# Kernel tuning notes

Measured on AMD Instinct MI355X. Metric: run time of the kernel, lower is better.

## Reference

```python
import jax, jax.numpy as jnp
import numpy as np

EPS = 1e-6  # LayerNorm epsilon


def setup_inputs() -> dict:
    key = jax.random.key(0)
    ks = jax.random.split(key, 12)
    B, S, T, E = 8, 2048, 2048, 512
    sc = 1.0 / np.sqrt(E)
    inp = {
        "encoder_outputs": jax.random.normal(ks[0], (B, S, E), jnp.float32),
        "emotion": jax.random.normal(ks[1], (B, T, E), jnp.float32),
        "mask": jax.random.randint(ks[2], (B, S, T), 0, 2).astype(bool),
        "Wq": jax.random.normal(ks[3], (E, E), jnp.float32) * sc,
        "bq": jnp.zeros((E,), jnp.float32),
        "Wk": jax.random.normal(ks[4], (E, E), jnp.float32) * sc,
        "bk": jnp.zeros((E,), jnp.float32),
        "Wv": jax.random.normal(ks[5], (E, E), jnp.float32) * sc,
        "bv": jnp.zeros((E,), jnp.float32),
        "Wo": jax.random.normal(ks[6], (E, E), jnp.float32) * sc,
        "gamma": jnp.ones((E,), jnp.float32),
        "beta": jnp.zeros((E,), jnp.float32),
    }
    return inp


def reference(encoder_outputs, emotion, mask, Wq, bq, Wk, bk, Wv, bv, Wo, gamma, beta):
    # Linear projections (torch Linear: x @ W.T + b)
    q = encoder_outputs @ Wq.T + bq          # [B,S,E]
    k = emotion @ Wk.T + bk                  # [B,T,E]
    v = emotion @ Wv.T + bv                  # [B,T,E]
    logits = jnp.einsum("bse,bte->bst", q, k)  # [B,S,T]
    logits = jnp.where(mask, jnp.float32(-1e18), logits)
    weights = jax.nn.softmax(logits, axis=-1)   # dropout1 = identity (eval)
    contexts = jnp.einsum("bst,bte->bse", weights, v)
    attn = contexts @ Wo.T                   # output_linear, no bias
    attn = encoder_outputs + attn            # dropout2 = identity (eval)
    # LayerNorm (std-based, as in common hand-rolled LayerNorm)
    mean = attn.mean(-1, keepdims=True)
    std = attn.std(-1, keepdims=True)
    context = gamma * (attn - mean) / (std + EPS) + beta
    context = encoder_outputs + context      # dropout3 = identity (eval)
    return context
```

## Files before the change

kernel.cpp:

```cpp
#include <hip/hip_runtime.h>
#include <math.h>
#include <stdint.h>


#define BB 8
#define SS 2048
#define TT 2048
#define EE 512

typedef __attribute__((ext_vector_type(8))) short short8;
typedef __attribute__((ext_vector_type(4))) float f32x4;

__device__ __forceinline__ uint16_t f2bf(float f) {
  uint32_t u = __builtin_bit_cast(uint32_t, f);
  u += 0x7fffu + ((u >> 16) & 1u);
  return (uint16_t)(u >> 16);
}
__device__ __forceinline__ float bf2f(uint16_t h) {
  uint32_t u = ((uint32_t)h) << 16;
  return __builtin_bit_cast(float, u);
}

__device__ __forceinline__ size_t toff(int row, int col, int ld) {
  return (size_t)(row >> 4) * ((size_t)ld << 4) + ((size_t)(col >> 3) << 7)
       + ((row & 15) << 3) + (col & 7);
}

__device__ __forceinline__ void gld16(const void* g, void* l) {
  __builtin_amdgcn_global_load_lds(
      (const __attribute__((address_space(1))) void*)g,
      (__attribute__((address_space(3))) void*)l, 16, 0, 0);
}

template<int ASRC, int BSRC, int EPI, int WN>
__global__ __launch_bounds__(256, 2) void mgemm(
    const void* __restrict__ Ap, const void* __restrict__ Alo,
    const void* __restrict__ Bp, const void* __restrict__ Blo,
    void* __restrict__ Cp, void* __restrict__ C2,
    const float* __restrict__ bias, const float* __restrict__ resid,
    const int* __restrict__ mask, float* __restrict__ sZ,
    int K, int lda, int ldb, int ldc,
    size_t sA, size_t sB, size_t sC, size_t sM)
{
  constexpr bool ALOARR = (ASRC == 0);
  constexpr bool BLOARR = (BSRC == 0);
  constexpr bool T3     = (ASRC == 0) && (BSRC == 0);
  constexpr int  BN     = 32 * WN;
  constexpr int  ABYTES = ALOARR ? 16384 : 8192;
  constexpr int  BBYTES = BLOARR ? BN * 128 : BN * 64;

  __shared__ char smem[ABYTES + BBYTES];

  const int tid  = threadIdx.x;
  const int lane = tid & 63, wv = tid >> 6;
  const int z    = blockIdx.z;
  const int bm   = blockIdx.y * 128;
  const int bn   = blockIdx.x * BN;
  const int fr   = lane & 15;
  const int wm   = (wv & 1) * 64;
  const int wn   = (wv >> 1) * (16 * WN);

  const f32x4 zero = {0.f, 0.f, 0.f, 0.f};
  f32x4 acc[4][WN];
#pragma unroll
  for (int i = 0; i < 4; ++i)
#pragma unroll
    for (int j = 0; j < WN; ++j) acc[i][j] = zero;

  const size_t loff = (size_t)lane * 8;
  const uint16_t* gAh = (const uint16_t*)Ap + sA * z + (size_t)(bm >> 4) * 16 * lda + loff;
  const uint16_t* gAl = ALOARR ? (const uint16_t*)Alo + sA * z + (size_t)(bm >> 4) * 16 * lda + loff : nullptr;
  const uint16_t* gBh = (const uint16_t*)Bp + sB * z + (size_t)(bn >> 4) * 16 * ldb + loff;
  const uint16_t* gBl = BLOARR ? (const uint16_t*)Blo + sB * z + (size_t)(bn >> 4) * 16 * ldb + loff : nullptr;

  for (int k0 = 0; k0 < K; k0 += 32) {
    const size_t ka = (size_t)k0 * 16;
    __syncthreads();
#pragma unroll
    for (int t = 0; t < 2; ++t) { int s = wv + t * 4;
      gld16(gAh + (size_t)s * 16 * lda + ka, &smem[s * 1024]); }
    if constexpr (ALOARR) {
#pragma unroll
      for (int t = 0; t < 2; ++t) { int s = wv + t * 4;
        gld16(gAl + (size_t)s * 16 * lda + ka, &smem[8192 + s * 1024]); }
    }
#pragma unroll
    for (int t = 0; t < WN / 2; ++t) { int s = wv + t * 4;
      gld16(gBh + (size_t)s * 16 * ldb + ka, &smem[ABYTES + s * 1024]); }
    if constexpr (BLOARR) {
#pragma unroll
      for (int t = 0; t < WN / 2; ++t) { int s = wv + t * 4;
        gld16(gBl + (size_t)s * 16 * ldb + ka, &smem[ABYTES + BN * 64 + s * 1024]); }
    }
    __syncthreads();

    short8 ah[4], bh[WN], al_[4], bl_[WN];
#pragma unroll
    for (int i = 0; i < 4; ++i) {
      const char* p = smem + ((wm >> 4) + i) * 1024 + (lane << 4);
      ah[i] = *(const short8*)p;
      if constexpr (ALOARR) al_[i] = *(const short8*)(p + 8192);
    }
#pragma unroll
    for (int j = 0; j < WN; ++j) {
      const char* p = smem + ABYTES + ((wn >> 4) + j) * 1024 + (lane << 4);
      bh[j] = *(const short8*)p;
      if constexpr (BLOARR) bl_[j] = *(const short8*)(p + BN * 64);
    }
#pragma unroll
    for (int i = 0; i < 4; ++i)
#pragma unroll
      for (int j = 0; j < WN; ++j) {
        acc[i][j] = __builtin_amdgcn_mfma_f32_16x16x32_bf16(ah[i], bh[j], acc[i][j], 0, 0, 0);
        if constexpr (T3) {
          acc[i][j] = __builtin_amdgcn_mfma_f32_16x16x32_bf16(ah[i], bl_[j], acc[i][j], 0, 0, 0);
          acc[i][j] = __builtin_amdgcn_mfma_f32_16x16x32_bf16(al_[i], bh[j], acc[i][j], 0, 0, 0);
        }
      }
  }

  if constexpr (EPI == 5) {
#pragma unroll
    for (int i = 0; i < 4; ++i) {
      const int row0 = bm + wm + i * 16 + (lane >> 4) * 4;
#pragma unroll
      for (int g = 0; g < 4; ++g) {
        const int row = row0 + g;
        float rs = 0.f;
#pragma unroll
        for (int j = 0; j < WN; ++j) {
          const int col = bn + wn + j * 16 + fr;
          const bool msk = mask[sM * z + (size_t)row * ldc + col] != 0;
          const float e = msk ? 0.f : __expf(acc[i][j][g] - 60.0f);
          ((uint16_t*)Cp)[sC * z + toff(row, col, ldc)] = f2bf(e);
          rs += e;
        }
        rs += __shfl_xor(rs, 1);
        rs += __shfl_xor(rs, 2);
        rs += __shfl_xor(rs, 4);
        rs += __shfl_xor(rs, 8);
        if ((lane & 15) == 0) atomicAdd(&sZ[(size_t)z * SS + row], rs);
      }
    }
  } else {
#pragma unroll
    for (int i = 0; i < 4; ++i) {
      const int row0 = bm + wm + i * 16 + (lane >> 4) * 4;
#pragma unroll
      for (int g = 0; g < 4; ++g) {
        const int row = row0 + g;
        float invZ = 1.0f;
        if constexpr (EPI == 6) invZ = 1.0f / sZ[(size_t)z * SS + row];
#pragma unroll
        for (int j = 0; j < WN; ++j) {
          const int col = bn + wn + j * 16 + fr;
          float v = acc[i][j][g];
          if constexpr (EPI == 0) {
            const size_t ci = sC * z + toff(row, col, ldc);
            v += bias[col];
            uint16_t h = f2bf(v);
            ((uint16_t*)Cp)[ci] = h;
            ((uint16_t*)C2)[ci] = f2bf(v - bf2f(h));
          } else if constexpr (EPI == 1) {
            v += bias[row];
            ((uint16_t*)Cp)[sC * z + toff(row, col, ldc)] = f2bf(v);
          } else if constexpr (EPI == 4) {
            v += resid[(size_t)row * ldc + col];
            ((float*)Cp)[sC * z + (size_t)row * ldc + col] = v;
          } else {
            ((uint16_t*)Cp)[sC * z + toff(row, col, ldc)] = f2bf(v * invZ);
          }
        }
      }
    }
  }
}

__global__ __launch_bounds__(256) void split_tiled(
    const float* __restrict__ x, uint16_t* __restrict__ hi,
    uint16_t* __restrict__ lo)
{
  __shared__ uint16_t lh[256 * 8 + 16 * 8];
  __shared__ uint16_t ll[256 * 8 + 16 * 8];
  const int t   = threadIdx.x;
  const int seg = blockIdx.x >> 2, q = blockIdx.x & 3;

  const float* src = x + (size_t)(seg * 16 + (t >> 4)) * 512 + q * 128 + (t & 15) * 8;
  float4 a = *(const float4*)src;
  float4 b = *(const float4*)(src + 4);
  float v[8] = {a.x, a.y, a.z, a.w, b.x, b.y, b.z, b.w};

  const int slot = (t & 15) * 16 + (t >> 4);
  uint16_t* ph = lh + slot * 8 + (slot >> 4) * 8;
  uint16_t* pl = ll + slot * 8 + (slot >> 4) * 8;
#pragma unroll
  for (int e = 0; e < 8; ++e) {
    uint16_t h = f2bf(v[e]);
    ph[e] = h;
    pl[e] = f2bf(v[e] - bf2f(h));
  }
  __syncthreads();

  const uint16_t* qh = lh + t * 8 + (t >> 4) * 8;
  const uint16_t* ql = ll + t * 8 + (t >> 4) * 8;
  const size_t off = (size_t)seg * 8192 + (size_t)(q * 16 + (t >> 4)) * 128 + (t & 15) * 8;
  *(short8*)(hi + off) = *(const short8*)qh;
  *(short8*)(lo + off) = *(const short8*)ql;
}

__global__ __launch_bounds__(256) void ln_kernel(
    const float* __restrict__ X, const float* __restrict__ enc,
    const float* __restrict__ gamma, const float* __restrict__ beta,
    float* __restrict__ out)
{
  const int row = blockIdx.x * 4 + (threadIdx.x >> 6);
  const int lane = threadIdx.x & 63;
  const size_t base = (size_t)row * EE;
  const int o0 = lane * 4, o1 = 256 + lane * 4;

  float4 x0 = *(const float4*)(X + base + o0);
  float4 x1 = *(const float4*)(X + base + o1);
  float s = x0.x + x0.y + x0.z + x0.w + x1.x + x1.y + x1.z + x1.w;
#pragma unroll
  for (int off = 32; off > 0; off >>= 1) s += __shfl_xor(s, off);
  const float mean = s * (1.0f / 512.0f);

  float d[8] = {x0.x - mean, x0.y - mean, x0.z - mean, x0.w - mean,
                x1.x - mean, x1.y - mean, x1.z - mean, x1.w - mean};
  float s2 = 0.f;
#pragma unroll
  for (int i = 0; i < 8; ++i) s2 = fmaf(d[i], d[i], s2);
#pragma unroll
  for (int off = 32; off > 0; off >>= 1) s2 += __shfl_xor(s2, off);
  const float stdv = sqrtf(s2 * (1.0f / 512.0f));
  const float inv = 1.0f / (stdv + 1e-6f);

  float4 g0 = *(const float4*)(gamma + o0);
  float4 g1 = *(const float4*)(gamma + o1);
  float4 b0 = *(const float4*)(beta + o0);
  float4 b1 = *(const float4*)(beta + o1);
  float4 e0 = *(const float4*)(enc + base + o0);
  float4 e1 = *(const float4*)(enc + base + o1);

  float4 r0, r1;
  r0.x = e0.x + g0.x * d[0] * inv + b0.x;
  r0.y = e0.y + g0.y * d[1] * inv + b0.y;
  r0.z = e0.z + g0.z * d[2] * inv + b0.z;
  r0.w = e0.w + g0.w * d[3] * inv + b0.w;
  r1.x = e1.x + g1.x * d[4] * inv + b1.x;
  r1.y = e1.y + g1.y * d[5] * inv + b1.y;
  r1.z = e1.z + g1.z * d[6] * inv + b1.z;
  r1.w = e1.w + g1.w * d[7] * inv + b1.w;
  *(float4*)(out + base + o0) = r0;
  *(float4*)(out + base + o1) = r1;
}

extern "C" void kernel_launch(void* const* d_in, const int* in_sizes, int n_in,
                              void* d_out, int out_size, void* d_ws, size_t ws_size,
                              hipStream_t stream) {
  const float* enc   = (const float*)d_in[0];
  const float* emo   = (const float*)d_in[1];
  const int*   mask  = (const int*)d_in[2];
  const float* Wq    = (const float*)d_in[3];
  const float* bq    = (const float*)d_in[4];
  const float* Wk    = (const float*)d_in[5];
  const float* bk    = (const float*)d_in[6];
  const float* Wv    = (const float*)d_in[7];
  const float* bv    = (const float*)d_in[8];
  const float* Wo    = (const float*)d_in[9];
  const float* gamma = (const float*)d_in[10];
  const float* beta  = (const float*)d_in[11];
  float* out = (float*)d_out;
  char*  ws  = (char*)d_ws;

  const size_t SZ = (size_t)BB * SS * EE;
  size_t off = 0;
  uint16_t* enc_h = (uint16_t*)(ws + off); off += SZ * 2;
  uint16_t* enc_l = (uint16_t*)(ws + off); off += SZ * 2;
  uint16_t* emo_h = (uint16_t*)(ws + off); off += SZ * 2;
  uint16_t* emo_l = (uint16_t*)(ws + off); off += SZ * 2;
  uint16_t* q_hi  = (uint16_t*)(ws + off); off += SZ * 2;
  uint16_t* q_lo  = (uint16_t*)(ws + off); off += SZ * 2;
  uint16_t* k_hi  = (uint16_t*)(ws + off); off += SZ * 2;
  uint16_t* k_lo  = (uint16_t*)(ws + off); off += SZ * 2;
  uint16_t* vT    = (uint16_t*)(ws + off); off += SZ * 2;
  uint16_t* ctx   = (uint16_t*)(ws + off); off += SZ * 2;
  uint16_t* wq_h  = (uint16_t*)(ws + off); off += EE * EE * 2;
  uint16_t* wq_l  = (uint16_t*)(ws + off); off += EE * EE * 2;
  uint16_t* wk_h  = (uint16_t*)(ws + off); off += EE * EE * 2;
  uint16_t* wk_l  = (uint16_t*)(ws + off); off += EE * EE * 2;
  uint16_t* wv_h  = (uint16_t*)(ws + off); off += EE * EE * 2;
  uint16_t* wv_l  = (uint16_t*)(ws + off); off += EE * EE * 2;
  uint16_t* wo_h  = (uint16_t*)(ws + off); off += EE * EE * 2;
  uint16_t* wo_l  = (uint16_t*)(ws + off); off += EE * EE * 2;
  uint16_t* P_u   = (uint16_t*)(ws + off); off += (size_t)BB * SS * TT * 2;
  float*    sZ    = (float*)(ws + off);    off += (size_t)BB * SS * 4;

  const dim3 blk(256);

  split_tiled<<<dim3(128),  blk, 0, stream>>>(Wq, wq_h, wq_l);
  split_tiled<<<dim3(128),  blk, 0, stream>>>(Wk, wk_h, wk_l);
  split_tiled<<<dim3(128),  blk, 0, stream>>>(Wv, wv_h, wv_l);
  split_tiled<<<dim3(128),  blk, 0, stream>>>(Wo, wo_h, wo_l);
  split_tiled<<<dim3(4096), blk, 0, stream>>>(enc, enc_h, enc_l);
  split_tiled<<<dim3(4096), blk, 0, stream>>>(emo, emo_h, emo_l);
  hipMemsetAsync(sZ, 0, (size_t)BB * SS * 4, stream);

  mgemm<0, 0, 0, 4><<<dim3(4, 128, 1), blk, 0, stream>>>(
      enc_h, enc_l, wq_h, wq_l, q_hi, q_lo, bq, nullptr, nullptr, nullptr,
      EE, EE, EE, EE, 0, 0, 0, 0);
  mgemm<0, 0, 0, 4><<<dim3(4, 128, 1), blk, 0, stream>>>(
      emo_h, emo_l, wk_h, wk_l, k_hi, k_lo, bk, nullptr, nullptr, nullptr,
      EE, EE, EE, EE, 0, 0, 0, 0);
  mgemm<1, 1, 1, 4><<<dim3(128, 4, 1), blk, 0, stream>>>(
      wv_h, nullptr, emo_h, nullptr, vT, nullptr, bv, nullptr, nullptr, nullptr,
      EE, EE, EE, BB * TT, 0, 0, 0, 0);

  mgemm<0, 0, 5, 4><<<dim3(16, 16, 8), blk, 0, stream>>>(
      q_hi, q_lo, k_hi, k_lo, P_u, nullptr, nullptr, nullptr, mask, sZ,
      EE, EE, EE, TT,
      (size_t)SS * EE, (size_t)TT * EE, (size_t)SS * TT, (size_t)SS * TT);

  mgemm<1, 1, 6, 4><<<dim3(4, 16, 8), blk, 0, stream>>>(
      P_u, nullptr, vT, nullptr, ctx, nullptr, nullptr, nullptr, nullptr, sZ,
      TT, TT, BB * TT, EE,
      (size_t)SS * TT, (size_t)TT * 16, (size_t)SS * EE, 0);

  mgemm<1, 1, 4, 4><<<dim3(4, 128, 1), blk, 0, stream>>>(
      ctx, nullptr, wo_h, nullptr, out, nullptr, nullptr, enc, nullptr, nullptr,
      EE, EE, EE, EE, 0, 0, 0, 0);
  ln_kernel<<<dim3(BB * SS / 4), blk, 0, stream>>>(out, enc, gamma, beta, out);
}
```

Baseline: 577.9 us.

## Batch split and Q/K projection launches, drop K low-part term in logits

Merges the four weight-split launches into one kernel and the two activation-split launches into another. The Q and K projections become a single batched GEMM launch, with per-z bias selection, relying on the workspace buffers being laid out contiguously. The QK^T logits GEMM now uses two bf16 MFMA terms instead of three by dropping K's low part, which cuts MFMA work and K-lo loads in the largest GEMM. The cost is slightly lower logit precision and a dependency on the workspace layout.

```diff
diff --git a/kernel.cpp b/kernel.cpp
--- a/kernel.cpp
+++ b/kernel.cpp
@@ -37,7 +37,8 @@
     const void* __restrict__ Ap, const void* __restrict__ Alo,
     const void* __restrict__ Bp, const void* __restrict__ Blo,
     void* __restrict__ Cp, void* __restrict__ C2,
-    const float* __restrict__ bias, const float* __restrict__ resid,
+    const float* __restrict__ bias, const float* __restrict__ bias2,
+    const float* __restrict__ resid,
     const int* __restrict__ mask, float* __restrict__ sZ,
     int K, int lda, int ldb, int ldc,
     size_t sA, size_t sB, size_t sC, size_t sM)
@@ -45,6 +46,7 @@
   constexpr bool ALOARR = (ASRC == 0);
   constexpr bool BLOARR = (BSRC == 0);
   constexpr bool T3     = (ASRC == 0) && (BSRC == 0);
+  constexpr bool T2     = (ASRC == 0) && (BSRC == 1);
   constexpr int  BN     = 32 * WN;
   constexpr int  ABYTES = ALOARR ? 16384 : 8192;
   constexpr int  BBYTES = BLOARR ? BN * 128 : BN * 64;
@@ -114,6 +116,8 @@
         acc[i][j] = __builtin_amdgcn_mfma_f32_16x16x32_bf16(ah[i], bh[j], acc[i][j], 0, 0, 0);
         if constexpr (T3) {
           acc[i][j] = __builtin_amdgcn_mfma_f32_16x16x32_bf16(ah[i], bl_[j], acc[i][j], 0, 0, 0);
+          acc[i][j] = __builtin_amdgcn_mfma_f32_16x16x32_bf16(al_[i], bh[j], acc[i][j], 0, 0, 0);
+        } else if constexpr (T2) {
           acc[i][j] = __builtin_amdgcn_mfma_f32_16x16x32_bf16(al_[i], bh[j], acc[i][j], 0, 0, 0);
         }
       }
@@ -156,8 +160,9 @@
           const int col = bn + wn + j * 16 + fr;
           float v = acc[i][j][g];
           if constexpr (EPI == 0) {
+            const float* bp = (z == 0) ? bias : bias2;
             const size_t ci = sC * z + toff(row, col, ldc);
-            v += bias[col];
+            v += bp[col];
             uint16_t h = f2bf(v);
             ((uint16_t*)Cp)[ci] = h;
             ((uint16_t*)C2)[ci] = f2bf(v - bf2f(h));
@@ -176,14 +181,14 @@
   }
 }
 
-__global__ __launch_bounds__(256) void split_tiled(
+__device__ __forceinline__ void split_core(
     const float* __restrict__ x, uint16_t* __restrict__ hi,
-    uint16_t* __restrict__ lo)
+    uint16_t* __restrict__ lo, int bid)
 {
   __shared__ uint16_t lh[256 * 8 + 16 * 8];
   __shared__ uint16_t ll[256 * 8 + 16 * 8];
   const int t   = threadIdx.x;
-  const int seg = blockIdx.x >> 2, q = blockIdx.x & 3;
+  const int seg = bid >> 2, q = bid & 3;
 
   const float* src = x + (size_t)(seg * 16 + (t >> 4)) * 512 + q * 128 + (t & 15) * 8;
   float4 a = *(const float4*)src;
@@ -206,6 +211,26 @@
   const size_t off = (size_t)seg * 8192 + (size_t)(q * 16 + (t >> 4)) * 128 + (t & 15) * 8;
   *(short8*)(hi + off) = *(const short8*)qh;
   *(short8*)(lo + off) = *(const short8*)ql;
+}
+
+__global__ __launch_bounds__(256) void split_pair(
+    const float* __restrict__ x0, const float* __restrict__ x1,
+    uint16_t* __restrict__ hi, uint16_t* __restrict__ lo, size_t stride)
+{
+  const int sel = blockIdx.x >> 12;
+  const int bid = blockIdx.x & 4095;
+  split_core(sel ? x1 : x0, hi + sel * stride, lo + sel * stride, bid);
+}
+
+__global__ __launch_bounds__(256) void split_w4(
+    const float* __restrict__ x0, const float* __restrict__ x1,
+    const float* __restrict__ x2, const float* __restrict__ x3,
+    uint16_t* __restrict__ hi0, uint16_t* __restrict__ lo0, size_t stride)
+{
+  const int w   = blockIdx.x >> 7;
+  const int bid = blockIdx.x & 127;
+  const float* x = (w == 0) ? x0 : (w == 1) ? x1 : (w == 2) ? x2 : x3;
+  split_core(x, hi0 + w * stride, lo0 + w * stride, bid);
 }
 
 __global__ __launch_bounds__(256) void ln_kernel(
@@ -295,39 +320,35 @@
   uint16_t* wo_l  = (uint16_t*)(ws + off); off += EE * EE * 2;
   uint16_t* P_u   = (uint16_t*)(ws + off); off += (size_t)BB * SS * TT * 2;
   float*    sZ    = (float*)(ws + off);    off += (size_t)BB * SS * 4;
+  (void)k_lo; (void)wk_l; (void)wv_l; (void)wo_l;
 
   const dim3 blk(256);
 
-  split_tiled<<<dim3(128),  blk, 0, stream>>>(Wq, wq_h, wq_l);
-  split_tiled<<<dim3(128),  blk, 0, stream>>>(Wk, wk_h, wk_l);
-  split_tiled<<<dim3(128),  blk, 0, stream>>>(Wv, wv_h, wv_l);
-  split_tiled<<<dim3(128),  blk, 0, stream>>>(Wo, wo_h, wo_l);
-  split_tiled<<<dim3(4096), blk, 0, stream>>>(enc, enc_h, enc_l);
-  split_tiled<<<dim3(4096), blk, 0, stream>>>(emo, emo_h, emo_l);
+  split_w4<<<dim3(512), blk, 0, stream>>>(Wq, Wk, Wv, Wo, wq_h, wq_l,
+                                          (size_t)2 * EE * EE);
+  split_pair<<<dim3(8192), blk, 0, stream>>>(enc, emo, enc_h, enc_l,
+                                             (size_t)2 * SZ);
   hipMemsetAsync(sZ, 0, (size_t)BB * SS * 4, stream);
 
-  mgemm<0, 0, 0, 4><<<dim3(4, 128, 1), blk, 0, stream>>>(
-      enc_h, enc_l, wq_h, wq_l, q_hi, q_lo, bq, nullptr, nullptr, nullptr,
-      EE, EE, EE, EE, 0, 0, 0, 0);
-  mgemm<0, 0, 0, 4><<<dim3(4, 128, 1), blk, 0, stream>>>(
-      emo_h, emo_l, wk_h, wk_l, k_hi, k_lo, bk, nullptr, nullptr, nullptr,
-      EE, EE, EE, EE, 0, 0, 0, 0);
+  mgemm<0, 0, 0, 4><<<dim3(4, 128, 2), blk, 0, stream>>>(
+      enc_h, enc_l, wq_h, wq_l, q_hi, q_lo, bq, bk, nullptr, nullptr, nullptr,
+      EE, EE, EE, EE, 2 * SZ, (size_t)2 * EE * EE, 2 * SZ, 0);
   mgemm<1, 1, 1, 4><<<dim3(128, 4, 1), blk, 0, stream>>>(
-      wv_h, nullptr, emo_h, nullptr, vT, nullptr, bv, nullptr, nullptr, nullptr,
-      EE, EE, EE, BB * TT, 0, 0, 0, 0);
-
-  mgemm<0, 0, 5, 4><<<dim3(16, 16, 8), blk, 0, stream>>>(
-      q_hi, q_lo, k_hi, k_lo, P_u, nullptr, nullptr, nullptr, mask, sZ,
-      EE, EE, EE, TT,
+      wv_h, nullptr, emo_h, nullptr, vT, nullptr, bv, nullptr, nullptr,
+      nullptr, nullptr, EE, EE, EE, BB * TT, 0, 0, 0, 0);
+
+  mgemm<0, 1, 5, 4><<<dim3(16, 16, 8), blk, 0, stream>>>(
+      q_hi, q_lo, k_hi, nullptr, P_u, nullptr, nullptr, nullptr, nullptr,
+      mask, sZ, EE, EE, EE, TT,
       (size_t)SS * EE, (size_t)TT * EE, (size_t)SS * TT, (size_t)SS * TT);
 
   mgemm<1, 1, 6, 4><<<dim3(4, 16, 8), blk, 0, stream>>>(
-      P_u, nullptr, vT, nullptr, ctx, nullptr, nullptr, nullptr, nullptr, sZ,
-      TT, TT, BB * TT, EE,
+      P_u, nullptr, vT, nullptr, ctx, nullptr, nullptr, nullptr, nullptr,
+      nullptr, sZ, TT, TT, BB * TT, EE,
       (size_t)SS * TT, (size_t)TT * 16, (size_t)SS * EE, 0);
 
   mgemm<1, 1, 4, 4><<<dim3(4, 128, 1), blk, 0, stream>>>(
-      ctx, nullptr, wo_h, nullptr, out, nullptr, nullptr, enc, nullptr, nullptr,
-      EE, EE, EE, EE, 0, 0, 0, 0);
+      ctx, nullptr, wo_h, nullptr, out, nullptr, nullptr, nullptr, enc,
+      nullptr, nullptr, EE, EE, EE, EE, 0, 0, 0, 0);
   ln_kernel<<<dim3(BB * SS / 4), blk, 0, stream>>>(out, enc, gamma, beta, out);
 }
```

New measurement: 564.2 us. -2.4%, faster.
